# Optimization experiments

Hardware: AMD Instinct MI355X
Metric: run time of the kernel (lower is better)

Reference implementation:

```python
import jax, jax.numpy as jnp
import numpy as np

H = 32          # query heads
D = 128         # head_dim
THETA = 10000.0
NEG = -1e30


def _rope_cos_sin(positions, d):
    half = d // 2
    inv_freq = 1.0 / (THETA ** (jnp.arange(0, d, 2, dtype=jnp.float32) / d))  # [half]
    ang = positions.astype(jnp.float32)[:, None] * inv_freq[None, :]          # [B, half]
    return jnp.cos(ang), jnp.sin(ang)


def _apply_rope(x, cos, sin):
    # neox-style rotary on last dim; cos/sin broadcast over leading dims
    half = x.shape[-1] // 2
    x1, x2 = x[..., :half], x[..., half:]
    return jnp.concatenate([x1 * cos - x2 * sin, x2 * cos + x1 * sin], axis=-1)


def setup_inputs() -> dict:
    key = jax.random.key(0)
    ks = jax.random.split(key, 8)
    B, hidden = 64, 4096
    num_blocks, block_size, max_blocks = 16384, 16, 256
    hidden_states = jax.random.normal(ks[0], (B, hidden), dtype=jnp.float32)
    wqkv = jax.random.normal(ks[1], (hidden, (H + 2) * D), dtype=jnp.float32) * 0.02
    wdense = jax.random.normal(ks[2], (hidden, hidden), dtype=jnp.float32) * 0.02
    k_cache = jax.random.normal(ks[3], (num_blocks, block_size, D), dtype=jnp.float32)
    v_cache = jax.random.normal(ks[4], (num_blocks, block_size, D), dtype=jnp.float32)
    # each sequence owns a distinct set of 256 blocks
    block_tables = jnp.arange(B * max_blocks, dtype=jnp.int64).reshape(B, max_blocks)
    context_lens = jax.random.randint(ks[5], (B,), 1, max_blocks * block_size + 1).astype(jnp.int64)
    positions = context_lens - 1  # position of the new (current) token
    return {
        "hidden_states": hidden_states, "wqkv": wqkv, "wdense": wdense,
        "k_cache": k_cache, "v_cache": v_cache,
        "positions": positions, "block_tables": block_tables,
        "context_lens": context_lens,
    }


def reference(hidden_states, wqkv, wdense, k_cache, v_cache,
              positions, block_tables, context_lens):
    B = hidden_states.shape[0]
    block_size = k_cache.shape[1]
    scale = 1.0 / np.sqrt(D).astype(np.float32)

    # fused QKV projection (bias=False in Falcon-7B config)
    qkv = hidden_states @ wqkv                                  # [B,(H+2)*D]
    q = qkv[:, : H * D].reshape(B, H, D)
    k = qkv[:, H * D : (H + 1) * D]                             # [B,D]  (MQA, 1 kv head)
    v = qkv[:, (H + 1) * D :]                                   # [B,D]

    # rotary embedding on q and k at the current positions
    cos, sin = _rope_cos_sin(positions, D)                      # [B,D/2]
    q = _apply_rope(q, cos[:, None, :], sin[:, None, :])
    k = _apply_rope(k, cos, sin)

    # write the new token's k/v into the paged cache (scatter)
    rows = jnp.arange(B)
    blk = block_tables[rows, positions // block_size]           # [B]
    off = positions % block_size
    k_cache = k_cache.at[blk, off].set(k)
    v_cache = v_cache.at[blk, off].set(v)

    # paged gather: assemble each sequence's KV from its block table
    keys = k_cache[block_tables].reshape(B, -1, D)              # [B,L,D]
    vals = v_cache[block_tables].reshape(B, -1, D)
    L = keys.shape[1]

    scores = jnp.einsum('bhd,bld->bhl', q, keys) * scale        # [B,H,L]
    valid = jnp.arange(L)[None, :] < context_lens[:, None]      # [B,L]
    scores = jnp.where(valid[:, None, :], scores, NEG)
    probs = jax.nn.softmax(scores, axis=-1)
    attn = jnp.einsum('bhl,bld->bhd', probs, vals).reshape(B, H * D)

    return attn @ wdense                                        # [B,hidden]
```

## Files before the change

### kernel.cpp

```cpp
#include <hip/hip_runtime.h>
#include <hip/hip_bf16.h>
#include <cmath>

#define NHEADS 32
#define DIM 128
#define SPLITS 16
#define TILE 32
#define KSPLIT 16
#define QKV_N 4352
#define HID 4096

typedef __attribute__((ext_vector_type(4))) float f32x4;
typedef __attribute__((ext_vector_type(8))) short short8i;
typedef __attribute__((ext_vector_type(4))) short short4i;

__device__ __forceinline__ unsigned short f2bf(float x) {
  unsigned int b = __float_as_uint(x);
  return (unsigned short)((b + 0x7FFFu + ((b >> 16) & 1u)) >> 16);
}
__device__ __forceinline__ unsigned int pk2bf(float lo, float hi) {
  return (unsigned)f2bf(lo) | ((unsigned)f2bf(hi) << 16);
}

__device__ __forceinline__ f32x4 mfma16bf16(short4i a, short4i b, f32x4 c) {
#if __has_builtin(__builtin_amdgcn_mfma_f32_16x16x16bf16_1k)
  return __builtin_amdgcn_mfma_f32_16x16x16bf16_1k(a, b, c, 0, 0, 0);
#else
  asm volatile("v_mfma_f32_16x16x16_bf16 %0, %1, %2, %0"
               : "+v"(c) : "v"(a), "v"(b));
  return c;
#endif
}

__global__ __launch_bounds__(256, 4) void gemm64_mfma(
    const float* __restrict__ A, const float* __restrict__ W,
    float* __restrict__ P, int N, int K)
{
  __shared__ unsigned short Ab[64][40];
  __shared__ unsigned short Wt[64][40];
  const int t = threadIdx.x;
  const int w = t >> 6, lane = t & 63;
  const int l4 = lane >> 4, l16 = lane & 15;
  const int n0 = blockIdx.x * 64;
  const int KS = K / KSPLIT;
  const int kbase = blockIdx.y * KS;

  const int ar = t >> 2, akq = t & 3;
  const int bn = t & 63, bkq = t >> 6;

  f32x4 acc[4];
#pragma unroll
  for (int i = 0; i < 4; ++i) acc[i] = (f32x4){0.f, 0.f, 0.f, 0.f};

  float4 a0, a1;
  float bw[8];

#define GLOAD(KC)                                                          \
  {                                                                        \
    const float* ap = A + (size_t)ar * K + kbase + (KC) + akq * 8;         \
    a0 = *(const float4*)ap;                                               \
    a1 = *(const float4*)(ap + 4);                                         \
    const float* wp = W + (size_t)(kbase + (KC) + bkq * 8) * N + n0 + bn;  \
    _Pragma("unroll")                                                      \
    for (int j = 0; j < 8; ++j) bw[j] = wp[(size_t)j * N];                 \
  }

#define SWRITE                                                             \
  {                                                                        \
    unsigned int ua[4] = {pk2bf(a0.x, a0.y), pk2bf(a0.z, a0.w),            \
                          pk2bf(a1.x, a1.y), pk2bf(a1.z, a1.w)};           \
    *(float4*)&Ab[ar][akq * 8] = *(float4*)ua;                             \
    unsigned int ub[4] = {pk2bf(bw[0], bw[1]), pk2bf(bw[2], bw[3]),        \
                          pk2bf(bw[4], bw[5]), pk2bf(bw[6], bw[7])};       \
    *(float4*)&Wt[bn][bkq * 8] = *(float4*)ub;                             \
  }

  GLOAD(0);
  SWRITE;
  __syncthreads();

  for (int kc = 0; kc < KS; kc += 32) {
    const bool pre = (kc + 32 < KS);
    if (pre) GLOAD(kc + 32);

    const short8i af = *(const short8i*)&Ab[w * 16 + l16][l4 * 8];
#pragma unroll
    for (int nt = 0; nt < 4; ++nt) {
      const short8i bf = *(const short8i*)&Wt[nt * 16 + l16][l4 * 8];
      acc[nt] = __builtin_amdgcn_mfma_f32_16x16x32_bf16(af, bf, acc[nt], 0, 0, 0);
    }

    __syncthreads();
    if (pre) {
      SWRITE;
      __syncthreads();
    }
  }

  float* base = P + (size_t)blockIdx.y * 64 * N + n0;
#pragma unroll
  for (int nt = 0; nt < 4; ++nt)
#pragma unroll
    for (int r = 0; r < 4; ++r)
      base[(size_t)(w * 16 + l4 * 4 + r) * N + nt * 16 + l16] = acc[nt][r];
#undef GLOAD
#undef SWRITE
}

__global__ __launch_bounds__(256) void reduce_parts(
    const float* __restrict__ P, float* __restrict__ C, int total)
{
  const int i = (blockIdx.x * 256 + threadIdx.x) * 4;
  if (i >= total) return;
  float4 s = *(const float4*)(P + i);
#pragma unroll
  for (int k = 1; k < KSPLIT; ++k) {
    const float4 v = *(const float4*)(P + (size_t)k * total + i);
    s.x += v.x; s.y += v.y; s.z += v.z; s.w += v.w;
  }
  *(float4*)(C + i) = s;
}

__global__ __launch_bounds__(256) void rope_kernel(
    float* __restrict__ qkv, const int* __restrict__ positions)
{
  const int b = blockIdx.x;
  float* row = qkv + (size_t)b * QKV_N;
  const float pos = (float)positions[b];
  for (int it = threadIdx.x; it < 33 * 64; it += 256) {
    const int r = it >> 6, i = it & 63;
    float* x = row + (r < 32 ? r * DIM : HID);
    const float ex = (float)(2 * i) * (1.0f / 128.0f);
    const float inv = 1.0f / powf(10000.0f, ex);
    const float ang = pos * inv;
    const float c = cosf(ang), sn = sinf(ang);
    const float x1 = x[i], x2 = x[i + 64];
    x[i]      = x1 * c - x2 * sn;
    x[i + 64] = x2 * c + x1 * sn;
  }
}

__global__ __launch_bounds__(256, 4) void attn_kernel(
    const float* __restrict__ qkv,
    const float* __restrict__ k_cache, const float* __restrict__ v_cache,
    const int* __restrict__ block_tables, const int* __restrict__ context_lens,
    float* __restrict__ pm, float* __restrict__ pl, float* __restrict__ pacc)
{
  const int b = blockIdx.x, s = blockIdx.y;
  const int t = threadIdx.x;
  const int w = t >> 6, lane = t & 63;
  const int hq = w >> 1, pq = w & 1;
  const int l4 = lane >> 4, l16 = lane & 15;
  const int ctx = context_lens[b];
  const int pos = ctx - 1;
  const int chunk = (ctx + SPLITS - 1) / SPLITS;
  const int start = s * chunk;
  const int end = min(start + chunk, ctx);
  const int nt = (end > start) ? ((end - start + TILE - 1) / TILE) : 0;

  __shared__ unsigned short KbU[32 * 128];
  __shared__ unsigned short VtU[128 * 34];
  __shared__ float red[2][64][36];
  __shared__ int bt_lds[24];

  const float* qbase = qkv + (size_t)b * QKV_N;
  const int bt0 = start >> 4;
  if (t < 24) {
    const int idx = bt0 + t;
    bt_lds[t] = (idx < 256) ? block_tables[b * 256 + idx] : 0;
  }

  const float scale = 0.08838834764831845f;
  short8i qf[4];
  {
    const float* qp0 = qbase + (hq * 16 + l16) * DIM + l4 * 8;
#pragma unroll
    for (int ks = 0; ks < 4; ++ks) {
      const float4 a = *(const float4*)(qp0 + ks * 32);
      const float4 c = *(const float4*)(qp0 + ks * 32 + 4);
      short8i q;
      q[0] = (short)f2bf(a.x * scale); q[1] = (short)f2bf(a.y * scale);
      q[2] = (short)f2bf(a.z * scale); q[3] = (short)f2bf(a.w * scale);
      q[4] = (short)f2bf(c.x * scale); q[5] = (short)f2bf(c.y * scale);
      q[6] = (short)f2bf(c.z * scale); q[7] = (short)f2bf(c.w * scale);
      qf[ks] = q;
    }
  }

  f32x4 o2[8];
#pragma unroll
  for (int i = 0; i < 8; ++i) o2[i] = (f32x4){0.f, 0.f, 0.f, 0.f};
  float lh = 0.f;

  float4 kreg[4], vreg[4];
  const int tk_sub = t >> 5;
  const int tk_col = t & 31;

#define LOADREGS(T0)                                                     \
  {                                                                      \
    _Pragma("unroll")                                                    \
    for (int j = 0; j < 4; ++j) {                                        \
      int gp_ = (T0) + j * 8 + tk_sub;                                   \
      if (gp_ > pos) gp_ = pos;                                          \
      const float* kp;                                                   \
      if (gp_ == pos) kp = qbase + HID;                                  \
      else {                                                             \
        const int blk = bt_lds[(gp_ >> 4) - bt0];                        \
        kp = k_cache + ((size_t)blk * 16 + (gp_ & 15)) * DIM;            \
      }                                                                  \
      kreg[j] = *(const float4*)(kp + tk_col * 4);                       \
    }                                                                    \
    int gv = (T0) + tk_col;                                              \
    if (gv > pos) gv = pos;                                              \
    const float* vp;                                                     \
    if (gv == pos) vp = qbase + HID + DIM;                               \
    else {                                                               \
      const int blk = bt_lds[(gv >> 4) - bt0];                           \
      vp = v_cache + ((size_t)blk * 16 + (gv & 15)) * DIM;               \
    }                                                                    \
    _Pragma("unroll")                                                    \
    for (int j = 0; j < 4; ++j)                                          \
      vreg[j] = *(const float4*)(vp + tk_sub * 16 + j * 4);              \
  }

#define WRITE_TILE                                                                     \
  {                                                                                    \
    _Pragma("unroll")                                                                  \
    for (int j = 0; j < 4; ++j) {                                                      \
      const int pl_ = j * 8 + tk_sub;                                                  \
      const int up = (tk_col >> 1) ^ (pl_ & 15);                                       \
      unsigned int lo = pk2bf(kreg[j].x, kreg[j].y);                                   \
      unsigned int hi = pk2bf(kreg[j].z, kreg[j].w);                                   \
      unsigned int* dst = (unsigned int*)&KbU[pl_ * 128 + up * 8 + (tk_col & 1) * 4];  \
      dst[0] = lo; dst[1] = hi;                                                        \
    }                                                                                  \
    _Pragma("unroll")                                                                  \
    for (int j = 0; j < 4; ++j) {                                                      \
      const int od0 = tk_sub * 16 + j * 4;                                             \
      VtU[(od0 + 0) * 34 + tk_col] = f2bf(vreg[j].x);                                  \
      VtU[(od0 + 1) * 34 + tk_col] = f2bf(vreg[j].y);                                  \
      VtU[(od0 + 2) * 34 + tk_col] = f2bf(vreg[j].z);                                  \
      VtU[(od0 + 3) * 34 + tk_col] = f2bf(vreg[j].w);                                  \
    }                                                                                  \
  }

  if (nt > 0) {
    __syncthreads();
    LOADREGS(start);
    WRITE_TILE;
    __syncthreads();

    for (int it = 0; it < nt; ++it) {
      const int t0 = start + it * TILE;
      const bool pre = (it + 1 < nt);
      if (pre) LOADREGS(t0 + TILE);

      f32x4 accs = {0.f, 0.f, 0.f, 0.f};
      const int rowK = pq * 16 + l16;
#pragma unroll
      for (int ks = 0; ks < 4; ++ks) {
        const int up = (l4 + ks * 4) ^ l16;
        const short8i kf = *(const short8i*)&KbU[rowK * 128 + up * 8];
        accs = __builtin_amdgcn_mfma_f32_16x16x32_bf16(kf, qf[ks], accs, 0, 0, 0);
      }

      const int pb_ = t0 + pq * 16 + l4 * 4;
      const float p0 = (pb_ + 0 < end) ? __expf(accs[0]) : 0.f;
      const float p1 = (pb_ + 1 < end) ? __expf(accs[1]) : 0.f;
      const float p2 = (pb_ + 2 < end) ? __expf(accs[2]) : 0.f;
      const float p3 = (pb_ + 3 < end) ? __expf(accs[3]) : 0.f;
      lh += (p0 + p1) + (p2 + p3);
      union { unsigned int u[2]; short4i v; } pc;
      pc.u[0] = pk2bf(p0, p1);
      pc.u[1] = pk2bf(p2, p3);
      const short4i pf = pc.v;

      const int vb = pq * 16 + l4 * 4;
#pragma unroll
      for (int ob = 0; ob < 8; ++ob) {
        const int rowV = ob * 16 + l16;
        union { unsigned int u[2]; short4i v; } vc;
        vc.u[0] = *(const unsigned int*)&VtU[rowV * 34 + vb];
        vc.u[1] = *(const unsigned int*)&VtU[rowV * 34 + vb + 2];
        o2[ob] = mfma16bf16(pf, vc.v, o2[ob]);
      }

      if (pre) {
        __syncthreads();
        WRITE_TILE;
        __syncthreads();
      }
    }
  }

  float lhr = lh;
  lhr += __shfl_xor(lhr, 16);
  lhr += __shfl_xor(lhr, 32);

  if (pq == 1) {
#pragma unroll
    for (int ob = 0; ob < 8; ++ob) *(f32x4*)&red[hq][lane][ob * 4] = o2[ob];
    red[hq][lane][32] = lhr;
  }
  __syncthreads();
  if (pq == 0) {
#pragma unroll
    for (int ob = 0; ob < 8; ++ob) {
      const f32x4 r4 = *(const f32x4*)&red[hq][lane][ob * 4];
      o2[ob] += r4;
    }
    lhr += red[hq][lane][32];
    const size_t sbase = (size_t)(b * SPLITS + s) * NHEADS + hq * 16;
#pragma unroll
    for (int ob = 0; ob < 8; ++ob) {
      pacc[(sbase + l4 * 4 + 0) * DIM + ob * 16 + l16] = o2[ob][0];
      pacc[(sbase + l4 * 4 + 1) * DIM + ob * 16 + l16] = o2[ob][1];
      pacc[(sbase + l4 * 4 + 2) * DIM + ob * 16 + l16] = o2[ob][2];
      pacc[(sbase + l4 * 4 + 3) * DIM + ob * 16 + l16] = o2[ob][3];
    }
    if (lane < 16) { pm[sbase + lane] = 0.f; pl[sbase + lane] = lhr; }
  }
#undef LOADREGS
#undef WRITE_TILE
}

__global__ __launch_bounds__(128) void combine_kernel(
    const float* __restrict__ pm, const float* __restrict__ pl,
    const float* __restrict__ pacc, float* __restrict__ attn)
{
  const int bh = blockIdx.x;
  const int b = bh >> 5, h = bh & 31;
  const int d = threadIdx.x;
  float ms[SPLITS], ls[SPLITS];
  float M = -1e30f;
#pragma unroll
  for (int s = 0; s < SPLITS; ++s) {
    ms[s] = pm[(size_t)(b * SPLITS + s) * NHEADS + h];
    ls[s] = pl[(size_t)(b * SPLITS + s) * NHEADS + h];
    M = fmaxf(M, ms[s]);
  }
  float L = 0.f, o = 0.f;
#pragma unroll
  for (int s = 0; s < SPLITS; ++s) {
    const float wgt = __expf(ms[s] - M);
    L += ls[s] * wgt;
    o += wgt * pacc[((size_t)(b * SPLITS + s) * NHEADS + h) * DIM + d];
  }
  attn[(size_t)b * HID + h * DIM + d] = o / L;
}

extern "C" void kernel_launch(void* const* d_in, const int* in_sizes, int n_in,
                              void* d_out, int out_size, void* d_ws, size_t ws_size,
                              hipStream_t stream) {
  const float* hidden   = (const float*)d_in[0];
  const float* wqkv     = (const float*)d_in[1];
  const float* wdense   = (const float*)d_in[2];
  const float* k_cache  = (const float*)d_in[3];
  const float* v_cache  = (const float*)d_in[4];
  const int* positions    = (const int*)d_in[5];
  const int* block_tables = (const int*)d_in[6];
  const int* context_lens = (const int*)d_in[7];
  float* out = (float*)d_out;

  float* qkv  = (float*)d_ws;
  float* attn = qkv + 64 * QKV_N;
  float* un   = attn + 64 * HID;
  float* gp   = un;
  float* pacc = un;
  float* pm   = pacc + (size_t)64 * SPLITS * NHEADS * DIM;
  float* pl   = pm + 64 * SPLITS * NHEADS;

  gemm64_mfma<<<dim3(QKV_N / 64, KSPLIT), 256, 0, stream>>>(hidden, wqkv, gp, QKV_N, HID);
  reduce_parts<<<(64 * QKV_N) / 1024, 256, 0, stream>>>(gp, qkv, 64 * QKV_N);
  rope_kernel<<<64, 256, 0, stream>>>(qkv, positions);
  attn_kernel<<<dim3(64, SPLITS), 256, 0, stream>>>(qkv, k_cache, v_cache,
                                                    block_tables, context_lens, pm, pl, pacc);
  combine_kernel<<<64 * NHEADS, 128, 0, stream>>>(pm, pl, pacc, attn);
  gemm64_mfma<<<dim3(HID / 64, KSPLIT), 256, 0, stream>>>(attn, wdense, gp, HID, HID);
  reduce_parts<<<(64 * HID) / 1024, 256, 0, stream>>>(gp, out, 64 * HID);
}
```

Baseline: 103.8 us.

## Load K/V fragments directly from global into registers, dropping LDS staging

The attention kernel no longer stages K and V tiles through shared memory with register prefetch and two barriers per tile. Each wave now loads its own K rows and V columns straight from the paged cache into registers, converts them to bf16 and feeds the MFMAs. This removes LDS traffic and per-tile synchronisation, but drops the software prefetch. V reads become scalar per-lane gathers that are less coalesced, and launch bounds are lowered to 3 waves, which allows more registers. The bf16 conversion also switches to the HIP intrinsic.

```diff
diff --git a/kernel.cpp b/kernel.cpp
--- a/kernel.cpp
+++ b/kernel.cpp
@@ -15,8 +15,8 @@
 typedef __attribute__((ext_vector_type(4))) short short4i;
 
 __device__ __forceinline__ unsigned short f2bf(float x) {
-  unsigned int b = __float_as_uint(x);
-  return (unsigned short)((b + 0x7FFFu + ((b >> 16) & 1u)) >> 16);
+  __hip_bfloat16 h = __float2bfloat16(x);
+  return *reinterpret_cast<unsigned short*>(&h);
 }
 __device__ __forceinline__ unsigned int pk2bf(float lo, float hi) {
   return (unsigned)f2bf(lo) | ((unsigned)f2bf(hi) << 16);
@@ -140,7 +140,7 @@
   }
 }
 
-__global__ __launch_bounds__(256, 4) void attn_kernel(
+__global__ __launch_bounds__(256, 3) void attn_kernel(
     const float* __restrict__ qkv,
     const float* __restrict__ k_cache, const float* __restrict__ v_cache,
     const int* __restrict__ block_tables, const int* __restrict__ context_lens,
@@ -158,8 +158,6 @@
   const int end = min(start + chunk, ctx);
   const int nt = (end > start) ? ((end - start + TILE - 1) / TILE) : 0;
 
-  __shared__ unsigned short KbU[32 * 128];
-  __shared__ unsigned short VtU[128 * 34];
   __shared__ float red[2][64][36];
   __shared__ int bt_lds[24];
 
@@ -169,6 +167,7 @@
     const int idx = bt0 + t;
     bt_lds[t] = (idx < 256) ? block_tables[b * 256 + idx] : 0;
   }
+  __syncthreads();
 
   const float scale = 0.08838834764831845f;
   short8i qf[4];
@@ -178,12 +177,12 @@
     for (int ks = 0; ks < 4; ++ks) {
       const float4 a = *(const float4*)(qp0 + ks * 32);
       const float4 c = *(const float4*)(qp0 + ks * 32 + 4);
-      short8i q;
-      q[0] = (short)f2bf(a.x * scale); q[1] = (short)f2bf(a.y * scale);
-      q[2] = (short)f2bf(a.z * scale); q[3] = (short)f2bf(a.w * scale);
-      q[4] = (short)f2bf(c.x * scale); q[5] = (short)f2bf(c.y * scale);
-      q[6] = (short)f2bf(c.z * scale); q[7] = (short)f2bf(c.w * scale);
-      qf[ks] = q;
+      union { unsigned int u[4]; short8i v; } qc;
+      qc.u[0] = pk2bf(a.x * scale, a.y * scale);
+      qc.u[1] = pk2bf(a.z * scale, a.w * scale);
+      qc.u[2] = pk2bf(c.x * scale, c.y * scale);
+      qc.u[3] = pk2bf(c.z * scale, c.w * scale);
+      qf[ks] = qc.v;
     }
   }
 
@@ -192,104 +191,74 @@
   for (int i = 0; i < 8; ++i) o2[i] = (f32x4){0.f, 0.f, 0.f, 0.f};
   float lh = 0.f;
 
-  float4 kreg[4], vreg[4];
-  const int tk_sub = t >> 5;
-  const int tk_col = t & 31;
-
-#define LOADREGS(T0)                                                     \
-  {                                                                      \
-    _Pragma("unroll")                                                    \
-    for (int j = 0; j < 4; ++j) {                                        \
-      int gp_ = (T0) + j * 8 + tk_sub;                                   \
-      if (gp_ > pos) gp_ = pos;                                          \
-      const float* kp;                                                   \
-      if (gp_ == pos) kp = qbase + HID;                                  \
-      else {                                                             \
-        const int blk = bt_lds[(gp_ >> 4) - bt0];                        \
-        kp = k_cache + ((size_t)blk * 16 + (gp_ & 15)) * DIM;            \
-      }                                                                  \
-      kreg[j] = *(const float4*)(kp + tk_col * 4);                       \
-    }                                                                    \
-    int gv = (T0) + tk_col;                                              \
-    if (gv > pos) gv = pos;                                              \
-    const float* vp;                                                     \
-    if (gv == pos) vp = qbase + HID + DIM;                               \
-    else {                                                               \
-      const int blk = bt_lds[(gv >> 4) - bt0];                           \
-      vp = v_cache + ((size_t)blk * 16 + (gv & 15)) * DIM;               \
-    }                                                                    \
-    _Pragma("unroll")                                                    \
-    for (int j = 0; j < 4; ++j)                                          \
-      vreg[j] = *(const float4*)(vp + tk_sub * 16 + j * 4);              \
-  }
-
-#define WRITE_TILE                                                                     \
-  {                                                                                    \
-    _Pragma("unroll")                                                                  \
-    for (int j = 0; j < 4; ++j) {                                                      \
-      const int pl_ = j * 8 + tk_sub;                                                  \
-      const int up = (tk_col >> 1) ^ (pl_ & 15);                                       \
-      unsigned int lo = pk2bf(kreg[j].x, kreg[j].y);                                   \
-      unsigned int hi = pk2bf(kreg[j].z, kreg[j].w);                                   \
-      unsigned int* dst = (unsigned int*)&KbU[pl_ * 128 + up * 8 + (tk_col & 1) * 4];  \
-      dst[0] = lo; dst[1] = hi;                                                        \
-    }                                                                                  \
-    _Pragma("unroll")                                                                  \
-    for (int j = 0; j < 4; ++j) {                                                      \
-      const int od0 = tk_sub * 16 + j * 4;                                             \
-      VtU[(od0 + 0) * 34 + tk_col] = f2bf(vreg[j].x);                                  \
-      VtU[(od0 + 1) * 34 + tk_col] = f2bf(vreg[j].y);                                  \
-      VtU[(od0 + 2) * 34 + tk_col] = f2bf(vreg[j].z);                                  \
-      VtU[(od0 + 3) * 34 + tk_col] = f2bf(vreg[j].w);                                  \
-    }                                                                                  \
-  }
-
-  if (nt > 0) {
-    __syncthreads();
-    LOADREGS(start);
-    WRITE_TILE;
-    __syncthreads();
-
-    for (int it = 0; it < nt; ++it) {
-      const int t0 = start + it * TILE;
-      const bool pre = (it + 1 < nt);
-      if (pre) LOADREGS(t0 + TILE);
-
-      f32x4 accs = {0.f, 0.f, 0.f, 0.f};
-      const int rowK = pq * 16 + l16;
-#pragma unroll
-      for (int ks = 0; ks < 4; ++ks) {
-        const int up = (l4 + ks * 4) ^ l16;
-        const short8i kf = *(const short8i*)&KbU[rowK * 128 + up * 8];
-        accs = __builtin_amdgcn_mfma_f32_16x16x32_bf16(kf, qf[ks], accs, 0, 0, 0);
-      }
-
-      const int pb_ = t0 + pq * 16 + l4 * 4;
-      const float p0 = (pb_ + 0 < end) ? __expf(accs[0]) : 0.f;
-      const float p1 = (pb_ + 1 < end) ? __expf(accs[1]) : 0.f;
-      const float p2 = (pb_ + 2 < end) ? __expf(accs[2]) : 0.f;
-      const float p3 = (pb_ + 3 < end) ? __expf(accs[3]) : 0.f;
-      lh += (p0 + p1) + (p2 + p3);
-      union { unsigned int u[2]; short4i v; } pc;
-      pc.u[0] = pk2bf(p0, p1);
-      pc.u[1] = pk2bf(p2, p3);
-      const short4i pf = pc.v;
-
-      const int vb = pq * 16 + l4 * 4;
-#pragma unroll
-      for (int ob = 0; ob < 8; ++ob) {
-        const int rowV = ob * 16 + l16;
-        union { unsigned int u[2]; short4i v; } vc;
-        vc.u[0] = *(const unsigned int*)&VtU[rowV * 34 + vb];
-        vc.u[1] = *(const unsigned int*)&VtU[rowV * 34 + vb + 2];
-        o2[ob] = mfma16bf16(pf, vc.v, o2[ob]);
-      }
-
-      if (pre) {
-        __syncthreads();
-        WRITE_TILE;
-        __syncthreads();
-      }
+  for (int it = 0; it < nt; ++it) {
+    const int t0 = start + it * TILE + pq * 16;
+
+    int kpos = t0 + l16;
+    if (kpos > pos) kpos = pos;
+    const float* kp;
+    if (kpos == pos) kp = qbase + HID;
+    else {
+      const int blk = bt_lds[(kpos >> 4) - bt0];
+      kp = k_cache + ((size_t)blk * 16 + (kpos & 15)) * DIM;
+    }
+    float4 kraw[8];
+#pragma unroll
+    for (int ks = 0; ks < 4; ++ks) {
+      kraw[ks * 2 + 0] = *(const float4*)(kp + ks * 32 + l4 * 8);
+      kraw[ks * 2 + 1] = *(const float4*)(kp + ks * 32 + l4 * 8 + 4);
+    }
+
+    const float *vp0, *vp1, *vp2, *vp3;
+#define VPTR(J, VP)                                                        \
+    {                                                                      \
+      int gv = t0 + l4 * 4 + (J);                                          \
+      if (gv > pos) gv = pos;                                              \
+      if (gv == pos) VP = qbase + HID + DIM;                               \
+      else {                                                               \
+        const int blk = bt_lds[(gv >> 4) - bt0];                           \
+        VP = v_cache + ((size_t)blk * 16 + (gv & 15)) * DIM;               \
+      }                                                                    \
+    }
+    VPTR(0, vp0) VPTR(1, vp1) VPTR(2, vp2) VPTR(3, vp3)
+#undef VPTR
+    float vraw[8][4];
+#pragma unroll
+    for (int ob = 0; ob < 8; ++ob) {
+      vraw[ob][0] = vp0[ob * 16 + l16];
+      vraw[ob][1] = vp1[ob * 16 + l16];
+      vraw[ob][2] = vp2[ob * 16 + l16];
+      vraw[ob][3] = vp3[ob * 16 + l16];
+    }
+
+    f32x4 accs = {0.f, 0.f, 0.f, 0.f};
+#pragma unroll
+    for (int ks = 0; ks < 4; ++ks) {
+      union { unsigned int u[4]; short8i v; } kc;
+      kc.u[0] = pk2bf(kraw[ks * 2].x,     kraw[ks * 2].y);
+      kc.u[1] = pk2bf(kraw[ks * 2].z,     kraw[ks * 2].w);
+      kc.u[2] = pk2bf(kraw[ks * 2 + 1].x, kraw[ks * 2 + 1].y);
+      kc.u[3] = pk2bf(kraw[ks * 2 + 1].z, kraw[ks * 2 + 1].w);
+      accs = __builtin_amdgcn_mfma_f32_16x16x32_bf16(kc.v, qf[ks], accs, 0, 0, 0);
+    }
+
+    const int pb_ = t0 + l4 * 4;
+    const float p0 = (pb_ + 0 < end) ? __expf(accs[0]) : 0.f;
+    const float p1 = (pb_ + 1 < end) ? __expf(accs[1]) : 0.f;
+    const float p2 = (pb_ + 2 < end) ? __expf(accs[2]) : 0.f;
+    const float p3 = (pb_ + 3 < end) ? __expf(accs[3]) : 0.f;
+    lh += (p0 + p1) + (p2 + p3);
+    union { unsigned int u[2]; short4i v; } pc;
+    pc.u[0] = pk2bf(p0, p1);
+    pc.u[1] = pk2bf(p2, p3);
+    const short4i pf = pc.v;
+
+#pragma unroll
+    for (int ob = 0; ob < 8; ++ob) {
+      union { unsigned int u[2]; short4i v; } vc;
+      vc.u[0] = pk2bf(vraw[ob][0], vraw[ob][1]);
+      vc.u[1] = pk2bf(vraw[ob][2], vraw[ob][3]);
+      o2[ob] = mfma16bf16(pf, vc.v, o2[ob]);
     }
   }
 
@@ -320,8 +289,6 @@
     }
     if (lane < 16) { pm[sbase + lane] = 0.f; pl[sbase + lane] = lhr; }
   }
-#undef LOADREGS
-#undef WRITE_TILE
 }
 
 __global__ __launch_bounds__(128) void combine_kernel(
```

After: 115.4 us. 1.11x slower.
